# Optimization experiments

Hardware: AMD Instinct MI355X
Metric: run time of the kernel (lower is better)

The kernel has to match this reference:

```python
import jax, jax.numpy as jnp
import numpy as np

N, C_IN, H, W = 64, 8, 256, 256
E = 4      # edge_emb_dim
D = 4      # node_emb_dim
K = 3      # kernel_size
DN = ('NCHW', 'OIHW', 'NCHW')


def conv2d(x, w, b, padding):
    y = jax.lax.conv_general_dilated(x, w, (1, 1), padding, dimension_numbers=DN)
    return y + b[None, :, None, None]


def _w(key, shape):
    fan_in = shape[1] * shape[2] * shape[3]
    return jax.random.normal(key, shape, dtype=jnp.float32) / np.sqrt(fan_in)


def setup_inputs() -> dict:
    key = jax.random.key(0)
    ks = jax.random.split(key, 16)
    return {
        'x': jax.random.normal(ks[0], (N, C_IN, H, W), dtype=jnp.float32),
        # downsampling: 1x1 conv C_IN -> E (kernel=stride=downsampling_factor=1)
        'w_down': _w(ks[1], (E, C_IN, 1, 1)), 'b_down': jnp.zeros((E,), jnp.float32),
        # edge network phi: two conv3x3 (E->E) each followed by silu
        'w_e1': _w(ks[2], (E, E, K, K)), 'b_e1': jnp.zeros((E,), jnp.float32),
        'w_e2': _w(ks[3], (E, E, K, K)), 'b_e2': jnp.zeros((E,), jnp.float32),
        # upsampling: ConvTranspose with kernel=stride=1 == 1x1 conv E -> E
        'w_up': _w(ks[4], (E, E, 1, 1)), 'b_up': jnp.zeros((E,), jnp.float32),
        # node network psi: conv3x3 (C_IN+E -> D), silu, conv3x3 (D -> D)
        'w_n1': _w(ks[5], (D, C_IN + E, K, K)), 'b_n1': jnp.zeros((D,), jnp.float32),
        'w_n2': _w(ks[6], (D, D, K, K)), 'b_n2': jnp.zeros((D,), jnp.float32),
        # pre_resid: 1x1 conv C_IN -> D (since in_channels != node_emb_dim)
        'w_r': _w(ks[7], (D, C_IN, 1, 1)), 'b_r': jnp.zeros((D,), jnp.float32),
    }


def reference(x, w_down, b_down, w_e1, b_e1, w_e2, b_e2, w_up, b_up,
              w_n1, b_n1, w_n2, b_n2, w_r, b_r):
    # vmap(downsampling)(x): treat cell axis N as conv batch. (N,E,H,W)
    z = conv2d(x, w_down, b_down, 'VALID')
    # cell-wise edge CNN phi
    h = jax.nn.silu(conv2d(z, w_e1, b_e1, 'SAME'))
    h = jax.nn.silu(conv2d(h, w_e2, b_e2, 'SAME'))
    # sum-aggregate over cells -> A: (E,H,W)
    A = h.sum(axis=0)
    # upsampling (kernel=stride=1 transpose conv == 1x1 conv); pad is a no-op here
    A = conv2d(A[None], w_up, b_up, 'VALID')[0]
    # node update: concat [x, A] on channels, cell-interaction CNN psi
    y = jnp.concatenate([x, jnp.broadcast_to(A[None], (N, E, H, W))], axis=1)
    y = jax.nn.silu(conv2d(y, w_n1, b_n1, 'SAME'))
    y = conv2d(y, w_n2, b_n2, 'SAME')
    # residual with channel-matching 1x1 conv
    y = y + conv2d(x, w_r, b_r, 'VALID')
    return y
```

## Files before the change

### kernel.cpp

```cpp
#include <hip/hip_runtime.h>
#include <hip/hip_bf16.h>

#define NCELL 64
#define CIN 8
#define EE 4
#define DD 4
#define HH 256
#define WW 256

#define EBH 32
#define NBH 26
#define NBANDS_E (HH / EBH)
#define NBANDS_N ((HH + NBH - 1) / NBH)
#define NSTRIP 5

__device__ __forceinline__ float4 f4z() { return make_float4(0.f, 0.f, 0.f, 0.f); }
__device__ __forceinline__ float silu1(float v) { return v / (1.0f + __expf(-v)); }
__device__ __forceinline__ float4 silu4f(const float a[4]) {
    return make_float4(silu1(a[0]), silu1(a[1]), silu1(a[2]), silu1(a[3]));
}
__device__ __forceinline__ float4 shfL(float4 v) {
    return make_float4(__shfl_up(v.x, 1), __shfl_up(v.y, 1),
                       __shfl_up(v.z, 1), __shfl_up(v.w, 1));
}
__device__ __forceinline__ float4 shfR(float4 v) {
    return make_float4(__shfl_down(v.x, 1), __shfl_down(v.y, 1),
                       __shfl_down(v.z, 1), __shfl_down(v.w, 1));
}

#define COMP(v,i) ((i)==0?(v).x:(i)==1?(v).y:(i)==2?(v).z:(v).w)

__device__ __forceinline__ void conv_group(const float4* L, const float4* C, const float4* R,
                                           const float* __restrict__ w, int ostride, int ibase,
                                           float acc[4]) {
#pragma unroll
    for (int dy = 0; dy < 3; ++dy) {
#pragma unroll
        for (int ci = 0; ci < 4; ++ci) {
            const float aL = COMP(L[dy], ci);
            const float aC = COMP(C[dy], ci);
            const float aR = COMP(R[dy], ci);
#pragma unroll
            for (int o = 0; o < 4; ++o) {
                const int base = o * ostride + (ibase + ci) * 9 + dy * 3;
                acc[o] = fmaf(aL, w[base + 0], acc[o]);
                acc[o] = fmaf(aC, w[base + 1], acc[o]);
                acc[o] = fmaf(aR, w[base + 2], acc[o]);
            }
        }
    }
}

__global__ __launch_bounds__(256) void edge_kernel(
    const float* __restrict__ x,
    const float* __restrict__ w_down, const float* __restrict__ b_down,
    const float* __restrict__ w_e1, const float* __restrict__ b_e1,
    const float* __restrict__ w_e2, const float* __restrict__ b_e2,
    float4* __restrict__ P)
{
    const int lane = threadIdx.x & 63;
    const int wv = threadIdx.x >> 6;
    const int y0 = blockIdx.x * EBH;
    const int s = blockIdx.y;
    const int n = blockIdx.z * 4 + wv;
    const int cx = s * 60 + lane - 2;
    const bool colok = (unsigned)cx < (unsigned)WW;
    const bool payload = (lane >= 2) && (lane < 62) && colok;
    const float* __restrict__ xn = x + (size_t)n * CIN * HH * WW;

    const float bd0 = b_down[0], bd1 = b_down[1], bd2 = b_down[2], bd3 = b_down[3];
    const float be10 = b_e1[0], be11 = b_e1[1], be12 = b_e1[2], be13 = b_e1[3];
    const float be20 = b_e2[0], be21 = b_e2[1], be22 = b_e2[2], be23 = b_e2[3];

    float4 za0 = f4z(), za1 = f4z(), za2 = f4z();
    float4 zb0 = f4z(), zb1 = f4z(), zb2 = f4z();
    float4 zc0 = f4z(), zc1 = f4z(), zc2 = f4z();
    float4 ha0 = f4z(), ha1 = f4z(), ha2 = f4z();
    float4 hb0 = f4z(), hb1 = f4z(), hb2 = f4z();
    float4 hc0 = f4z(), hc1 = f4z(), hc2 = f4z();

    for (int k = 0; k < EBH + 4; ++k) {
        const int zr = y0 - 2 + k;

        float4 zn = f4z();
        if ((unsigned)zr < (unsigned)HH) {
            if (colok) {
                float a0 = bd0, a1 = bd1, a2 = bd2, a3 = bd3;
#pragma unroll
                for (int i = 0; i < CIN; ++i) {
                    const float xv = xn[((size_t)i * HH + zr) * WW + cx];
                    a0 = fmaf(xv, w_down[0 * CIN + i], a0);
                    a1 = fmaf(xv, w_down[1 * CIN + i], a1);
                    a2 = fmaf(xv, w_down[2 * CIN + i], a2);
                    a3 = fmaf(xv, w_down[3 * CIN + i], a3);
                }
                zn = make_float4(a0, a1, a2, a3);
            }
        }
        za0 = za1; za1 = za2; za2 = zn;
        zb0 = zb1; zb1 = zb2; zb2 = shfL(zn);
        zc0 = zc1; zc1 = zc2; zc2 = shfR(zn);

        if (k >= 2) {
            float acc[4] = { be10, be11, be12, be13 };
            {
                float4 L[3] = { zb0, zb1, zb2 };
                float4 C[3] = { za0, za1, za2 };
                float4 R[3] = { zc0, zc1, zc2 };
                conv_group(L, C, R, w_e1, 36, 0, acc);
            }
            const int hr = zr - 1;
            const float4 hn = ((unsigned)hr < (unsigned)HH && colok) ? silu4f(acc) : f4z();
            ha0 = ha1; ha1 = ha2; ha2 = hn;
            hb0 = hb1; hb1 = hb2; hb2 = shfL(hn);
            hc0 = hc1; hc1 = hc2; hc2 = shfR(hn);
        }

        if (k >= 4) {
            float acc[4] = { be20, be21, be22, be23 };
            {
                float4 L[3] = { hb0, hb1, hb2 };
                float4 C[3] = { ha0, ha1, ha2 };
                float4 R[3] = { hc0, hc1, hc2 };
                conv_group(L, C, R, w_e2, 36, 0, acc);
            }
            if (payload) {
                const int orow = zr - 2;
                P[(size_t)n * (HH * WW) + orow * WW + cx] = silu4f(acc);
            }
        }
    }
}

__global__ __launch_bounds__(256) void reduce_kernel(
    const float4* __restrict__ P, float4* __restrict__ A4)
{
    const int p = blockIdx.x * 256 + threadIdx.x;
    float4 a = f4z(), b = f4z(), c = f4z(), d = f4z();
#pragma unroll
    for (int nn = 0; nn < NCELL; nn += 4) {
        const float4 v0 = P[(size_t)(nn + 0) * (HH * WW) + p];
        const float4 v1 = P[(size_t)(nn + 1) * (HH * WW) + p];
        const float4 v2 = P[(size_t)(nn + 2) * (HH * WW) + p];
        const float4 v3 = P[(size_t)(nn + 3) * (HH * WW) + p];
        a.x += v0.x; a.y += v0.y; a.z += v0.z; a.w += v0.w;
        b.x += v1.x; b.y += v1.y; b.z += v1.z; b.w += v1.w;
        c.x += v2.x; c.y += v2.y; c.z += v2.z; c.w += v2.w;
        d.x += v3.x; d.y += v3.y; d.z += v3.z; d.w += v3.w;
    }
    A4[p] = make_float4(a.x + b.x + c.x + d.x, a.y + b.y + c.y + d.y,
                        a.z + b.z + c.z + d.z, a.w + b.w + c.w + d.w);
}

__global__ __launch_bounds__(256) void node_kernel(
    const float* __restrict__ x, const float* __restrict__ A,
    const float* __restrict__ w_up, const float* __restrict__ b_up,
    const float* __restrict__ w_n1, const float* __restrict__ b_n1,
    const float* __restrict__ w_n2, const float* __restrict__ b_n2,
    const float* __restrict__ w_r, const float* __restrict__ b_r,
    float* __restrict__ out)
{
    const int lane = threadIdx.x & 63;
    const int wv = threadIdx.x >> 6;
    const int y0 = blockIdx.x * NBH;
    const int h = min(NBH, HH - y0);
    const int s = blockIdx.y;
    const int n = blockIdx.z * 4 + wv;
    const int cx = s * 60 + lane - 2;
    const bool colok = (unsigned)cx < (unsigned)WW;
    const bool payload = (lane >= 2) && (lane < 62) && colok;
    const float* __restrict__ xn = x + (size_t)n * CIN * HH * WW;
    const float4* __restrict__ A4 = reinterpret_cast<const float4*>(A);

    const float bu0 = b_up[0], bu1 = b_up[1], bu2 = b_up[2], bu3 = b_up[3];
    const float bn10 = b_n1[0], bn11 = b_n1[1], bn12 = b_n1[2], bn13 = b_n1[3];
    const float br0 = b_n2[0] + b_r[0], br1 = b_n2[1] + b_r[1];
    const float br2 = b_n2[2] + b_r[2], br3 = b_n2[3] + b_r[3];

    float4 sa[3][3];
#pragma unroll
    for (int g = 0; g < 3; ++g) { sa[g][0] = f4z(); sa[g][1] = f4z(); sa[g][2] = f4z(); }
    float4 ya[3] = { f4z(), f4z(), f4z() };
    float4 yb[3] = { f4z(), f4z(), f4z() };
    float4 yc[3] = { f4z(), f4z(), f4z() };

    for (int k = 0; k < h + 4; ++k) {
        const int zr = y0 - 2 + k;

        float4 Sn0 = f4z(), Sn1 = f4z(), Sn2 = f4z();
        if ((unsigned)zr < (unsigned)HH) {
            if (colok) {
                float xv[CIN];
#pragma unroll
                for (int i = 0; i < CIN; ++i) xv[i] = xn[((size_t)i * HH + zr) * WW + cx];
                Sn0 = make_float4(xv[0], xv[1], xv[2], xv[3]);
                Sn1 = make_float4(xv[4], xv[5], xv[6], xv[7]);
                const float4 a4 = A4[zr * WW + cx];
                float u0 = bu0, u1 = bu1, u2 = bu2, u3 = bu3;
#pragma unroll
                for (int e = 0; e < 4; ++e) {
                    const float av = COMP(a4, e);
                    u0 = fmaf(av, w_up[0 * EE + e], u0);
                    u1 = fmaf(av, w_up[1 * EE + e], u1);
                    u2 = fmaf(av, w_up[2 * EE + e], u2);
                    u3 = fmaf(av, w_up[3 * EE + e], u3);
                }
                Sn2 = make_float4(u0, u1, u2, u3);
            }
        }
        sa[0][0] = sa[0][1]; sa[0][1] = sa[0][2]; sa[0][2] = Sn0;
        sa[1][0] = sa[1][1]; sa[1][1] = sa[1][2]; sa[1][2] = Sn1;
        sa[2][0] = sa[2][1]; sa[2][1] = sa[2][2]; sa[2][2] = Sn2;

        if (k >= 2) {
            float acc[4] = { bn10, bn11, bn12, bn13 };
#pragma unroll
            for (int g = 0; g < 3; ++g) {
                float4 L[3] = { shfL(sa[g][0]), shfL(sa[g][1]), shfL(sa[g][2]) };
                float4 R[3] = { shfR(sa[g][0]), shfR(sa[g][1]), shfR(sa[g][2]) };
                conv_group(L, sa[g], R, w_n1, 108, 4 * g, acc);
            }
            const int hr = zr - 1;
            const float4 yn = ((unsigned)hr < (unsigned)HH && colok) ? silu4f(acc) : f4z();
            ya[0] = ya[1]; ya[1] = ya[2]; ya[2] = yn;
            yb[0] = yb[1]; yb[1] = yb[2]; yb[2] = shfL(yn);
            yc[0] = yc[1]; yc[1] = yc[2]; yc[2] = shfR(yn);
        }

        if (k >= 4) {
            float acc[4] = { br0, br1, br2, br3 };
            conv_group(yb, ya, yc, w_n2, 36, 0, acc);
#pragma unroll
            for (int g = 0; g < 2; ++g) {
                const float4 xr = (g == 0) ? sa[0][0] : sa[1][0];
#pragma unroll
                for (int ci = 0; ci < 4; ++ci) {
                    const float a = COMP(xr, ci);
                    acc[0] = fmaf(a, w_r[0 * CIN + g * 4 + ci], acc[0]);
                    acc[1] = fmaf(a, w_r[1 * CIN + g * 4 + ci], acc[1]);
                    acc[2] = fmaf(a, w_r[2 * CIN + g * 4 + ci], acc[2]);
                    acc[3] = fmaf(a, w_r[3 * CIN + g * 4 + ci], acc[3]);
                }
            }
            if (payload) {
                const int orow = zr - 2;
#pragma unroll
                for (int o = 0; o < 4; ++o)
                    out[(((size_t)n * DD + o) * HH + orow) * WW + cx] = acc[o];
            }
        }
    }
}

extern "C" void kernel_launch(void* const* d_in, const int* in_sizes, int n_in,
                              void* d_out, int out_size, void* d_ws, size_t ws_size,
                              hipStream_t stream) {
    const float* x      = (const float*)d_in[0];
    const float* w_down = (const float*)d_in[1];
    const float* b_down = (const float*)d_in[2];
    const float* w_e1   = (const float*)d_in[3];
    const float* b_e1   = (const float*)d_in[4];
    const float* w_e2   = (const float*)d_in[5];
    const float* b_e2   = (const float*)d_in[6];
    const float* w_up   = (const float*)d_in[7];
    const float* b_up   = (const float*)d_in[8];
    const float* w_n1   = (const float*)d_in[9];
    const float* b_n1   = (const float*)d_in[10];
    const float* w_n2   = (const float*)d_in[11];
    const float* b_n2   = (const float*)d_in[12];
    const float* w_r    = (const float*)d_in[13];
    const float* b_r    = (const float*)d_in[14];
    float* out = (float*)d_out;

    float4* P = (float4*)d_out;
    float* A  = (float*)d_ws;

    edge_kernel<<<dim3(NBANDS_E, NSTRIP, NCELL / 4), dim3(256), 0, stream>>>(
        x, w_down, b_down, w_e1, b_e1, w_e2, b_e2, P);

    reduce_kernel<<<dim3(HH * WW / 256), dim3(256), 0, stream>>>(P, (float4*)A);

    node_kernel<<<dim3(NBANDS_N, NSTRIP, NCELL / 4), dim3(256), 0, stream>>>(
        x, A, w_up, b_up, w_n1, b_n1, w_n2, b_n2, w_r, b_r, out);
}
```

Before: 311.5 us.

## Scatter conv rows into rolling accumulators, shrink bands, split reduce across cells

The edge and node kernels now scatter each new input row into three rolling output-row accumulators instead of keeping three-row sliding windows of inputs. This cuts the live register state and the repeated shuffles per row. Band heights drop to 16 rows for both kernels, giving more blocks but more halo recompute. The reduce kernel splits the 64-cell sum across four waves and combines the partial sums in shared memory, which gives more parallelism per pixel.

```diff
diff --git a/kernel.cpp b/kernel.cpp
--- a/kernel.cpp
+++ b/kernel.cpp
@@ -8,16 +8,18 @@
 #define HH 256
 #define WW 256
 
-#define EBH 32
-#define NBH 26
+#define EBH 16
+#define NBH 16
 #define NBANDS_E (HH / EBH)
-#define NBANDS_N ((HH + NBH - 1) / NBH)
+#define NBANDS_N (HH / NBH)
 #define NSTRIP 5
+
+#define COMP(v,i) ((i)==0?(v).x:(i)==1?(v).y:(i)==2?(v).z:(v).w)
 
 __device__ __forceinline__ float4 f4z() { return make_float4(0.f, 0.f, 0.f, 0.f); }
 __device__ __forceinline__ float silu1(float v) { return v / (1.0f + __expf(-v)); }
-__device__ __forceinline__ float4 silu4f(const float a[4]) {
-    return make_float4(silu1(a[0]), silu1(a[1]), silu1(a[2]), silu1(a[3]));
+__device__ __forceinline__ float4 silu4(float4 v) {
+    return make_float4(silu1(v.x), silu1(v.y), silu1(v.z), silu1(v.w));
 }
 __device__ __forceinline__ float4 shfL(float4 v) {
     return make_float4(__shfl_up(v.x, 1), __shfl_up(v.y, 1),
@@ -27,27 +29,23 @@
     return make_float4(__shfl_down(v.x, 1), __shfl_down(v.y, 1),
                        __shfl_down(v.z, 1), __shfl_down(v.w, 1));
 }
-
-#define COMP(v,i) ((i)==0?(v).x:(i)==1?(v).y:(i)==2?(v).z:(v).w)
-
-__device__ __forceinline__ void conv_group(const float4* L, const float4* C, const float4* R,
-                                           const float* __restrict__ w, int ostride, int ibase,
-                                           float acc[4]) {
-#pragma unroll
-    for (int dy = 0; dy < 3; ++dy) {
-#pragma unroll
-        for (int ci = 0; ci < 4; ++ci) {
-            const float aL = COMP(L[dy], ci);
-            const float aC = COMP(C[dy], ci);
-            const float aR = COMP(R[dy], ci);
-#pragma unroll
-            for (int o = 0; o < 4; ++o) {
-                const int base = o * ostride + (ibase + ci) * 9 + dy * 3;
-                acc[o] = fmaf(aL, w[base + 0], acc[o]);
-                acc[o] = fmaf(aC, w[base + 1], acc[o]);
-                acc[o] = fmaf(aR, w[base + 2], acc[o]);
-            }
-        }
+__device__ __forceinline__ void fma4s(float4& a, float s, const float* __restrict__ w,
+                                      int ostride, int idx) {
+    a.x = fmaf(s, w[0 * ostride + idx], a.x);
+    a.y = fmaf(s, w[1 * ostride + idx], a.y);
+    a.z = fmaf(s, w[2 * ostride + idx], a.z);
+    a.w = fmaf(s, w[3 * ostride + idx], a.w);
+}
+
+__device__ __forceinline__ void contrib3(float4 Lv, float4 Cv, float4 Rv,
+                                         const float* __restrict__ w, int ostride,
+                                         int ibase, int dy, float4& acc) {
+#pragma unroll
+    for (int ci = 0; ci < 4; ++ci) {
+        const int idx = (ibase + ci) * 9 + dy * 3;
+        fma4s(acc, COMP(Lv, ci), w, ostride, idx + 0);
+        fma4s(acc, COMP(Cv, ci), w, ostride, idx + 1);
+        fma4s(acc, COMP(Rv, ci), w, ostride, idx + 2);
     }
 }
 
@@ -68,88 +66,77 @@
     const bool payload = (lane >= 2) && (lane < 62) && colok;
     const float* __restrict__ xn = x + (size_t)n * CIN * HH * WW;
 
-    const float bd0 = b_down[0], bd1 = b_down[1], bd2 = b_down[2], bd3 = b_down[3];
-    const float be10 = b_e1[0], be11 = b_e1[1], be12 = b_e1[2], be13 = b_e1[3];
-    const float be20 = b_e2[0], be21 = b_e2[1], be22 = b_e2[2], be23 = b_e2[3];
-
-    float4 za0 = f4z(), za1 = f4z(), za2 = f4z();
-    float4 zb0 = f4z(), zb1 = f4z(), zb2 = f4z();
-    float4 zc0 = f4z(), zc1 = f4z(), zc2 = f4z();
-    float4 ha0 = f4z(), ha1 = f4z(), ha2 = f4z();
-    float4 hb0 = f4z(), hb1 = f4z(), hb2 = f4z();
-    float4 hc0 = f4z(), hc1 = f4z(), hc2 = f4z();
+    const float4 bdn = make_float4(b_down[0], b_down[1], b_down[2], b_down[3]);
+    const float4 be1 = make_float4(b_e1[0], b_e1[1], b_e1[2], b_e1[3]);
+    const float4 be2 = make_float4(b_e2[0], b_e2[1], b_e2[2], b_e2[3]);
+
+    float4 hacc_a = f4z(), hacc_b = f4z();
+    float4 oacc_a = f4z(), oacc_b = f4z();
 
     for (int k = 0; k < EBH + 4; ++k) {
         const int zr = y0 - 2 + k;
 
         float4 zn = f4z();
-        if ((unsigned)zr < (unsigned)HH) {
-            if (colok) {
-                float a0 = bd0, a1 = bd1, a2 = bd2, a3 = bd3;
-#pragma unroll
-                for (int i = 0; i < CIN; ++i) {
-                    const float xv = xn[((size_t)i * HH + zr) * WW + cx];
-                    a0 = fmaf(xv, w_down[0 * CIN + i], a0);
-                    a1 = fmaf(xv, w_down[1 * CIN + i], a1);
-                    a2 = fmaf(xv, w_down[2 * CIN + i], a2);
-                    a3 = fmaf(xv, w_down[3 * CIN + i], a3);
-                }
-                zn = make_float4(a0, a1, a2, a3);
-            }
-        }
-        za0 = za1; za1 = za2; za2 = zn;
-        zb0 = zb1; zb1 = zb2; zb2 = shfL(zn);
-        zc0 = zc1; zc1 = zc2; zc2 = shfR(zn);
+        if ((unsigned)zr < (unsigned)HH && colok) {
+            zn = bdn;
+#pragma unroll
+            for (int i = 0; i < CIN; ++i) {
+                const float xv = xn[((size_t)i * HH + zr) * WW + cx];
+                zn.x = fmaf(xv, w_down[0 * CIN + i], zn.x);
+                zn.y = fmaf(xv, w_down[1 * CIN + i], zn.y);
+                zn.z = fmaf(xv, w_down[2 * CIN + i], zn.z);
+                zn.w = fmaf(xv, w_down[3 * CIN + i], zn.w);
+            }
+        }
+        const float4 zL = shfL(zn), zR = shfR(zn);
+
+        float4 hacc_c = be1;
+        contrib3(zL, zn, zR, w_e1, 36, 0, 0, hacc_c);
+        contrib3(zL, zn, zR, w_e1, 36, 0, 1, hacc_b);
+        contrib3(zL, zn, zR, w_e1, 36, 0, 2, hacc_a);
 
         if (k >= 2) {
-            float acc[4] = { be10, be11, be12, be13 };
-            {
-                float4 L[3] = { zb0, zb1, zb2 };
-                float4 C[3] = { za0, za1, za2 };
-                float4 R[3] = { zc0, zc1, zc2 };
-                conv_group(L, C, R, w_e1, 36, 0, acc);
-            }
             const int hr = zr - 1;
-            const float4 hn = ((unsigned)hr < (unsigned)HH && colok) ? silu4f(acc) : f4z();
-            ha0 = ha1; ha1 = ha2; ha2 = hn;
-            hb0 = hb1; hb1 = hb2; hb2 = shfL(hn);
-            hc0 = hc1; hc1 = hc2; hc2 = shfR(hn);
-        }
-
-        if (k >= 4) {
-            float acc[4] = { be20, be21, be22, be23 };
-            {
-                float4 L[3] = { hb0, hb1, hb2 };
-                float4 C[3] = { ha0, ha1, ha2 };
-                float4 R[3] = { hc0, hc1, hc2 };
-                conv_group(L, C, R, w_e2, 36, 0, acc);
-            }
-            if (payload) {
+            const float4 hn = ((unsigned)hr < (unsigned)HH && colok) ? silu4(hacc_a) : f4z();
+            const float4 hL = shfL(hn), hR = shfR(hn);
+            float4 oacc_c = be2;
+            contrib3(hL, hn, hR, w_e2, 36, 0, 0, oacc_c);
+            contrib3(hL, hn, hR, w_e2, 36, 0, 1, oacc_b);
+            contrib3(hL, hn, hR, w_e2, 36, 0, 2, oacc_a);
+
+            if (k >= 4 && payload) {
                 const int orow = zr - 2;
-                P[(size_t)n * (HH * WW) + orow * WW + cx] = silu4f(acc);
-            }
-        }
+                P[(size_t)n * (HH * WW) + orow * WW + cx] = silu4(oacc_a);
+            }
+            oacc_a = oacc_b; oacc_b = oacc_c;
+        }
+        hacc_a = hacc_b; hacc_b = hacc_c;
     }
 }
 
 __global__ __launch_bounds__(256) void reduce_kernel(
     const float4* __restrict__ P, float4* __restrict__ A4)
 {
-    const int p = blockIdx.x * 256 + threadIdx.x;
-    float4 a = f4z(), b = f4z(), c = f4z(), d = f4z();
-#pragma unroll
-    for (int nn = 0; nn < NCELL; nn += 4) {
-        const float4 v0 = P[(size_t)(nn + 0) * (HH * WW) + p];
-        const float4 v1 = P[(size_t)(nn + 1) * (HH * WW) + p];
-        const float4 v2 = P[(size_t)(nn + 2) * (HH * WW) + p];
-        const float4 v3 = P[(size_t)(nn + 3) * (HH * WW) + p];
+    __shared__ float4 buf[256];
+    const int tid = threadIdx.x;
+    const int pix = blockIdx.x * 64 + (tid & 63);
+    const int c0 = (tid >> 6) * 16;
+    float4 a = f4z(), b = f4z();
+#pragma unroll
+    for (int j = 0; j < 16; j += 2) {
+        const float4 v0 = P[(size_t)(c0 + j + 0) * (HH * WW) + pix];
+        const float4 v1 = P[(size_t)(c0 + j + 1) * (HH * WW) + pix];
         a.x += v0.x; a.y += v0.y; a.z += v0.z; a.w += v0.w;
         b.x += v1.x; b.y += v1.y; b.z += v1.z; b.w += v1.w;
-        c.x += v2.x; c.y += v2.y; c.z += v2.z; c.w += v2.w;
-        d.x += v3.x; d.y += v3.y; d.z += v3.z; d.w += v3.w;
-    }
-    A4[p] = make_float4(a.x + b.x + c.x + d.x, a.y + b.y + c.y + d.y,
-                        a.z + b.z + c.z + d.z, a.w + b.w + c.w + d.w);
+    }
+    buf[tid] = make_float4(a.x + b.x, a.y + b.y, a.z + b.z, a.w + b.w);
+    __syncthreads();
+    if (tid < 64) {
+        const float4 p0 = buf[tid], p1 = buf[tid + 64], p2 = buf[tid + 128], p3 = buf[tid + 192];
+        A4[blockIdx.x * 64 + tid] =
+            make_float4(p0.x + p1.x + p2.x + p3.x, p0.y + p1.y + p2.y + p3.y,
+                        p0.z + p1.z + p2.z + p3.z, p0.w + p1.w + p2.w + p3.w);
+    }
 }
 
 __global__ __launch_bounds__(256) void node_kernel(
@@ -163,7 +150,6 @@
     const int lane = threadIdx.x & 63;
     const int wv = threadIdx.x >> 6;
     const int y0 = blockIdx.x * NBH;
-    const int h = min(NBH, HH - y0);
     const int s = blockIdx.y;
     const int n = blockIdx.z * 4 + wv;
     const int cx = s * 60 + lane - 2;
@@ -172,83 +158,75 @@
     const float* __restrict__ xn = x + (size_t)n * CIN * HH * WW;
     const float4* __restrict__ A4 = reinterpret_cast<const float4*>(A);
 
-    const float bu0 = b_up[0], bu1 = b_up[1], bu2 = b_up[2], bu3 = b_up[3];
-    const float bn10 = b_n1[0], bn11 = b_n1[1], bn12 = b_n1[2], bn13 = b_n1[3];
-    const float br0 = b_n2[0] + b_r[0], br1 = b_n2[1] + b_r[1];
-    const float br2 = b_n2[2] + b_r[2], br3 = b_n2[3] + b_r[3];
-
-    float4 sa[3][3];
-#pragma unroll
-    for (int g = 0; g < 3; ++g) { sa[g][0] = f4z(); sa[g][1] = f4z(); sa[g][2] = f4z(); }
-    float4 ya[3] = { f4z(), f4z(), f4z() };
-    float4 yb[3] = { f4z(), f4z(), f4z() };
-    float4 yc[3] = { f4z(), f4z(), f4z() };
-
-    for (int k = 0; k < h + 4; ++k) {
+    const float4 bup = make_float4(b_up[0], b_up[1], b_up[2], b_up[3]);
+    const float4 bn1 = make_float4(b_n1[0], b_n1[1], b_n1[2], b_n1[3]);
+    const float4 bn2r = make_float4(b_n2[0] + b_r[0], b_n2[1] + b_r[1],
+                                    b_n2[2] + b_r[2], b_n2[3] + b_r[3]);
+
+    float4 yacc_a = f4z(), yacc_b = f4z();
+    float4 oacc_a = f4z(), oacc_b = f4z();
+
+    for (int k = 0; k < NBH + 4; ++k) {
         const int zr = y0 - 2 + k;
 
-        float4 Sn0 = f4z(), Sn1 = f4z(), Sn2 = f4z();
-        if ((unsigned)zr < (unsigned)HH) {
-            if (colok) {
-                float xv[CIN];
-#pragma unroll
-                for (int i = 0; i < CIN; ++i) xv[i] = xn[((size_t)i * HH + zr) * WW + cx];
-                Sn0 = make_float4(xv[0], xv[1], xv[2], xv[3]);
-                Sn1 = make_float4(xv[4], xv[5], xv[6], xv[7]);
-                const float4 a4 = A4[zr * WW + cx];
-                float u0 = bu0, u1 = bu1, u2 = bu2, u3 = bu3;
-#pragma unroll
-                for (int e = 0; e < 4; ++e) {
-                    const float av = COMP(a4, e);
-                    u0 = fmaf(av, w_up[0 * EE + e], u0);
-                    u1 = fmaf(av, w_up[1 * EE + e], u1);
-                    u2 = fmaf(av, w_up[2 * EE + e], u2);
-                    u3 = fmaf(av, w_up[3 * EE + e], u3);
-                }
-                Sn2 = make_float4(u0, u1, u2, u3);
-            }
-        }
-        sa[0][0] = sa[0][1]; sa[0][1] = sa[0][2]; sa[0][2] = Sn0;
-        sa[1][0] = sa[1][1]; sa[1][1] = sa[1][2]; sa[1][2] = Sn1;
-        sa[2][0] = sa[2][1]; sa[2][1] = sa[2][2]; sa[2][2] = Sn2;
+        float4 S0 = f4z(), S1 = f4z(), S2 = f4z();
+        if ((unsigned)zr < (unsigned)HH && colok) {
+            float xv[CIN];
+#pragma unroll
+            for (int i = 0; i < CIN; ++i) xv[i] = xn[((size_t)i * HH + zr) * WW + cx];
+            S0 = make_float4(xv[0], xv[1], xv[2], xv[3]);
+            S1 = make_float4(xv[4], xv[5], xv[6], xv[7]);
+            const float4 a4 = A4[zr * WW + cx];
+            S2 = bup;
+#pragma unroll
+            for (int e = 0; e < 4; ++e) {
+                const float av = COMP(a4, e);
+                S2.x = fmaf(av, w_up[0 * EE + e], S2.x);
+                S2.y = fmaf(av, w_up[1 * EE + e], S2.y);
+                S2.z = fmaf(av, w_up[2 * EE + e], S2.z);
+                S2.w = fmaf(av, w_up[3 * EE + e], S2.w);
+            }
+        }
+        const float4 L0 = shfL(S0), R0 = shfR(S0);
+        const float4 L1 = shfL(S1), R1 = shfR(S1);
+        const float4 L2 = shfL(S2), R2 = shfR(S2);
+
+        float4 yacc_c = bn1;
+        contrib3(L0, S0, R0, w_n1, 108, 0, 0, yacc_c);
+        contrib3(L1, S1, R1, w_n1, 108, 4, 0, yacc_c);
+        contrib3(L2, S2, R2, w_n1, 108, 8, 0, yacc_c);
+        contrib3(L0, S0, R0, w_n1, 108, 0, 1, yacc_b);
+        contrib3(L1, S1, R1, w_n1, 108, 4, 1, yacc_b);
+        contrib3(L2, S2, R2, w_n1, 108, 8, 1, yacc_b);
+        contrib3(L0, S0, R0, w_n1, 108, 0, 2, yacc_a);
+        contrib3(L1, S1, R1, w_n1, 108, 4, 2, yacc_a);
+        contrib3(L2, S2, R2, w_n1, 108, 8, 2, yacc_a);
 
         if (k >= 2) {
-            float acc[4] = { bn10, bn11, bn12, bn13 };
-#pragma unroll
-            for (int g = 0; g < 3; ++g) {
-                float4 L[3] = { shfL(sa[g][0]), shfL(sa[g][1]), shfL(sa[g][2]) };
-                float4 R[3] = { shfR(sa[g][0]), shfR(sa[g][1]), shfR(sa[g][2]) };
-                conv_group(L, sa[g], R, w_n1, 108, 4 * g, acc);
-            }
             const int hr = zr - 1;
-            const float4 yn = ((unsigned)hr < (unsigned)HH && colok) ? silu4f(acc) : f4z();
-            ya[0] = ya[1]; ya[1] = ya[2]; ya[2] = yn;
-            yb[0] = yb[1]; yb[1] = yb[2]; yb[2] = shfL(yn);
-            yc[0] = yc[1]; yc[1] = yc[2]; yc[2] = shfR(yn);
-        }
-
-        if (k >= 4) {
-            float acc[4] = { br0, br1, br2, br3 };
-            conv_group(yb, ya, yc, w_n2, 36, 0, acc);
-#pragma unroll
-            for (int g = 0; g < 2; ++g) {
-                const float4 xr = (g == 0) ? sa[0][0] : sa[1][0];
-#pragma unroll
-                for (int ci = 0; ci < 4; ++ci) {
-                    const float a = COMP(xr, ci);
-                    acc[0] = fmaf(a, w_r[0 * CIN + g * 4 + ci], acc[0]);
-                    acc[1] = fmaf(a, w_r[1 * CIN + g * 4 + ci], acc[1]);
-                    acc[2] = fmaf(a, w_r[2 * CIN + g * 4 + ci], acc[2]);
-                    acc[3] = fmaf(a, w_r[3 * CIN + g * 4 + ci], acc[3]);
-                }
-            }
-            if (payload) {
+            const float4 yn = ((unsigned)hr < (unsigned)HH && colok) ? silu4(yacc_a) : f4z();
+            const float4 yL = shfL(yn), yR = shfR(yn);
+
+            float4 oacc_c = bn2r;
+#pragma unroll
+            for (int ci = 0; ci < 4; ++ci) {
+                fma4s(oacc_c, COMP(S0, ci), w_r, CIN, ci);
+                fma4s(oacc_c, COMP(S1, ci), w_r, CIN, 4 + ci);
+            }
+            contrib3(yL, yn, yR, w_n2, 36, 0, 0, oacc_c);
+            contrib3(yL, yn, yR, w_n2, 36, 0, 1, oacc_b);
+            contrib3(yL, yn, yR, w_n2, 36, 0, 2, oacc_a);
+
+            if (k >= 4 && payload) {
                 const int orow = zr - 2;
-#pragma unroll
-                for (int o = 0; o < 4; ++o)
-                    out[(((size_t)n * DD + o) * HH + orow) * WW + cx] = acc[o];
-            }
-        }
+                out[(((size_t)n * DD + 0) * HH + orow) * WW + cx] = oacc_a.x;
+                out[(((size_t)n * DD + 1) * HH + orow) * WW + cx] = oacc_a.y;
+                out[(((size_t)n * DD + 2) * HH + orow) * WW + cx] = oacc_a.z;
+                out[(((size_t)n * DD + 3) * HH + orow) * WW + cx] = oacc_a.w;
+            }
+            oacc_a = oacc_b; oacc_b = oacc_c;
+        }
+        yacc_a = yacc_b; yacc_b = yacc_c;
     }
 }
 
@@ -278,7 +256,7 @@
     edge_kernel<<<dim3(NBANDS_E, NSTRIP, NCELL / 4), dim3(256), 0, stream>>>(
         x, w_down, b_down, w_e1, b_e1, w_e2, b_e2, P);
 
-    reduce_kernel<<<dim3(HH * WW / 256), dim3(256), 0, stream>>>(P, (float4*)A);
+    reduce_kernel<<<dim3(HH * WW / 64), dim3(256), 0, stream>>>(P, (float4*)A);
 
     node_kernel<<<dim3(NBANDS_N, NSTRIP, NCELL / 4), dim3(256), 0, stream>>>(
         x, A, w_up, b_up, w_n1, b_n1, w_n2, b_n2, w_r, b_r, out);
```

Result: slower. 545.7 us (+75.2%).
